# Kernel tuning notes

Measured on AMD Instinct MI355X. Metric: run time of the kernel, lower is better.

## Reference

```python
import jax, jax.numpy as jnp
import numpy as np

N_NODES = 50000
N_EDGES = 600000
HIDDEN = 128
INNER = 256


def _sage_pool(x, src, dst, Wp, bp, Wl, bl, Wr):
    # GraphSAGE 'pool' aggregator: max_j ReLU(W_pool x_j + b_pool) over in-neighbors,
    # then lin_l(aggregated) + lin_r(x_i). lin_l carries the bias (PyG convention).
    m = jax.nn.relu(x[src] @ Wp.T + bp)                      # [E, H] gather + transform
    agg = jax.ops.segment_max(m, dst, num_segments=x.shape[0])  # [N, H] scatter-max
    agg = jnp.where(jnp.isfinite(agg), agg, 0.0)             # isolated nodes -> 0
    return agg @ Wl.T + bl + x @ Wr.T


def setup_inputs() -> dict:
    key = jax.random.key(0)
    ks = jax.random.split(key, 16)
    s_h = 1.0 / np.sqrt(HIDDEN)
    x = jax.random.normal(ks[0], (N_NODES, HIDDEN), dtype=jnp.float32)
    edge_index = jax.random.randint(ks[1], (2, N_EDGES), 0, N_NODES, dtype=jnp.int64)
    p = {}
    # sage1
    p["Wp1"] = jax.random.normal(ks[2], (HIDDEN, HIDDEN), jnp.float32) * s_h
    p["bp1"] = jnp.zeros((HIDDEN,), jnp.float32)
    p["Wl1"] = jax.random.normal(ks[3], (HIDDEN, HIDDEN), jnp.float32) * s_h
    p["bl1"] = jnp.zeros((HIDDEN,), jnp.float32)
    p["Wr1"] = jax.random.normal(ks[4], (HIDDEN, HIDDEN), jnp.float32) * s_h
    # sage2
    p["Wp2"] = jax.random.normal(ks[5], (HIDDEN, HIDDEN), jnp.float32) * s_h
    p["bp2"] = jnp.zeros((HIDDEN,), jnp.float32)
    p["Wl2"] = jax.random.normal(ks[6], (HIDDEN, HIDDEN), jnp.float32) * s_h
    p["bl2"] = jnp.zeros((HIDDEN,), jnp.float32)
    p["Wr2"] = jax.random.normal(ks[7], (HIDDEN, HIDDEN), jnp.float32) * s_h
    # final linear hidden -> inner
    p["Wlin"] = jax.random.normal(ks[8], (INNER, HIDDEN), jnp.float32) * s_h
    p["blin"] = jnp.zeros((INNER,), jnp.float32)
    return {"x": x, "edge_index": edge_index, **p}


def reference(x, edge_index, Wp1, bp1, Wl1, bl1, Wr1, Wp2, bp2, Wl2, bl2, Wr2, Wlin, blin):
    src, dst = edge_index[0], edge_index[1]
    h = _sage_pool(x, src, dst, Wp1, bp1, Wl1, bl1, Wr1)
    h = jax.nn.gelu(h)
    h = _sage_pool(h, src, dst, Wp2, bp2, Wl2, bl2, Wr2)
    h = jax.nn.gelu(h)
    h = jax.nn.gelu(h @ Wlin.T + blin)
    return (h, edge_index)
```

## Files before the change

### kernel.cpp

```cpp
#include <hip/hip_runtime.h>

#define N_NODES 50000
#define N_EDGES 600000
#define HID 128

typedef __attribute__((ext_vector_type(8))) short short8;
typedef __attribute__((ext_vector_type(4))) float f32x4;

__device__ __forceinline__ unsigned short f2bf(float f) {
    unsigned u = __float_as_uint(f);
    unsigned r = u + 0x7FFFu + ((u >> 16) & 1u);
    return (unsigned short)(r >> 16);
}
__device__ __forceinline__ float bf2f(unsigned short h) {
    return __uint_as_float(((unsigned)h) << 16);
}

__device__ __forceinline__ float gelu_fast(float x) {
    float u = 0.7978845608028654f * (x + 0.044715f * x * x * x);
    return x / (1.0f + __expf(-2.0f * u));
}

__global__ void zero_deg(int* __restrict__ zbase) {
    int i = blockIdx.x * 256 + threadIdx.x;
    if (i < 12501) ((int4*)zbase)[i] = make_int4(0, 0, 0, 0);
}

#define CNT_BLOCKS  2344
#define CVT_BLOCKS  3125
#define PACK_BLOCKS 512
__global__ void prep(const float* __restrict__ x, unsigned short* __restrict__ xbf,
                     const float* __restrict__ Wp1, const float* __restrict__ Wl1,
                     const float* __restrict__ Wr1, const float* __restrict__ Wp2,
                     const float* __restrict__ Wl2, const float* __restrict__ Wr2,
                     const float* __restrict__ Wlin, unsigned short* __restrict__ wpack,
                     const int* __restrict__ ei, int* __restrict__ deg,
                     int* __restrict__ rank) {
    int b = blockIdx.x;
    if (b < CNT_BLOCKS) {
        int e = b * 256 + threadIdx.x;
        if (e < N_EDGES) {
            int dst = ei[N_EDGES + e];
            rank[e] = atomicAdd(&deg[dst], 1);
        }
    } else if (b < CNT_BLOCKS + CVT_BLOCKS) {
        int tid = (b - CNT_BLOCKS) * 256 + threadIdx.x;
        size_t i8 = (size_t)tid * 8;
        if (i8 >= (size_t)N_NODES * HID) return;
        float4 v0 = *(const float4*)(x + i8);
        float4 v1 = *(const float4*)(x + i8 + 4);
        short8 o;
        o[0] = f2bf(v0.x); o[1] = f2bf(v0.y); o[2] = f2bf(v0.z); o[3] = f2bf(v0.w);
        o[4] = f2bf(v1.x); o[5] = f2bf(v1.y); o[6] = f2bf(v1.z); o[7] = f2bf(v1.w);
        *(short8*)(xbf + i8) = o;
    } else {
        int pb = b - CNT_BLOCKS - CVT_BLOCKS;
        const float* W;
        int base, idx;
        if (pb < 384) {
            int which = pb >> 6;
            switch (which) {
                case 0: W = Wp1; break;
                case 1: W = Wl1; break;
                case 2: W = Wr1; break;
                case 3: W = Wp2; break;
                case 4: W = Wl2; break;
                default: W = Wr2; break;
            }
            base = which * 16384;
            idx = (pb & 63) * 256 + threadIdx.x;
        } else {
            W = Wlin;
            base = 98304;
            idx = (pb - 384) * 256 + threadIdx.x;
        }
        int j = idx & 7;
        int lane = (idx >> 3) & 63;
        int ks = (idx >> 9) & 3;
        int nt = idx >> 11;
        int c = nt * 16 + (lane & 15);
        int k = ks * 32 + (lane >> 4) * 8 + j;
        wpack[base + idx] = f2bf(W[c * 128 + k]);
    }
}

__global__ void build_off(const int* __restrict__ deg, int* __restrict__ off,
                          int* __restrict__ cursor) {
    __shared__ int sm[256];
    __shared__ int base;
    int t = threadIdx.x;
    int i = blockIdx.x * 256 + t;
    int v = (i < N_NODES) ? deg[i] : 0;
    sm[t] = v;
    __syncthreads();
    for (int s = 1; s < 256; s <<= 1) {
        int tv = (t >= s) ? sm[t - s] : 0;
        __syncthreads();
        sm[t] += tv;
        __syncthreads();
    }
    if (t == 255) base = atomicAdd(cursor, sm[255]);
    __syncthreads();
    if (i < N_NODES) off[i] = base + sm[t] - v;
}

#define FB   2344
#define EB4  1172
#define LB   1563
__global__ __launch_bounds__(256, 2) void combo(
        const int* __restrict__ ei, const int* __restrict__ off,
        const int* __restrict__ rank, int* __restrict__ csr,
        float* __restrict__ echo,
        const unsigned short* __restrict__ in1, const unsigned short* __restrict__ B1,
        const float* __restrict__ bias1, unsigned short* __restrict__ out1) {
    int b = blockIdx.x;
    int t = threadIdx.x;
    if (b < FB) {
        int e = b * 256 + t;
        if (e < N_EDGES) {
            int dst = ei[N_EDGES + e];
            csr[off[dst] + rank[e]] = ei[e];
        }
        return;
    }
    if (b < FB + EB4) {
        int idx = (b - FB) * 256 + t;
        int i = idx * 4;
        if (i < 2 * N_EDGES) {
            int4 v = *(const int4*)(ei + i);
            float4 f = make_float4((float)v.x, (float)v.y, (float)v.z, (float)v.w);
            *(float4*)(echo + i) = f;
        }
        return;
    }
    {
        __shared__ alignas(16) unsigned short hA[32][128];
        const int bid = b - FB - EB4;
        const int w = t >> 6;
        const int l = t & 63;
        const int blockRow = bid * 32;

        int r0 = blockRow + (l & 15);
        int r1 = r0 + 16;
        if (r0 > N_NODES - 1) r0 = N_NODES - 1;
        if (r1 > N_NODES - 1) r1 = N_NODES - 1;
        const int ko = (l >> 4) * 8;

        short8 a1[2][4];
#pragma unroll
        for (int ks = 0; ks < 4; ++ks) {
            a1[0][ks] = *(const short8*)(in1 + (size_t)r0 * HID + ks * 32 + ko);
            a1[1][ks] = *(const short8*)(in1 + (size_t)r1 * HID + ks * 32 + ko);
        }
        const int cL = l & 15;
        const int rfrag = (l >> 4) * 4;

        short8 b1v[8];
        const size_t gb = (size_t)(w * 8) * 64 + l;
#pragma unroll
        for (int s = 0; s < 8; ++s)
            b1v[s] = *(const short8*)(B1 + (gb + (size_t)s * 64) * 8);

#pragma unroll
        for (int m = 0; m < 2; ++m) {
            const int nt = w * 2 + m;
            f32x4 acc0 = {0.f, 0.f, 0.f, 0.f};
            f32x4 acc1 = {0.f, 0.f, 0.f, 0.f};
#pragma unroll
            for (int ks = 0; ks < 4; ++ks) {
                const int step = m * 4 + ks;
                acc0 = __builtin_amdgcn_mfma_f32_16x16x32_bf16(a1[0][ks], b1v[step], acc0, 0, 0, 0);
                acc1 = __builtin_amdgcn_mfma_f32_16x16x32_bf16(a1[1][ks], b1v[step], acc1, 0, 0, 0);
            }
            float bc = bias1[nt * 16 + cL];
#pragma unroll
            for (int reg = 0; reg < 4; ++reg) {
                int rl = rfrag + reg;
                int cs = (nt * 16 + cL) ^ ((rl & 7) << 3);
                hA[rl][cs] = f2bf(acc0[reg] + bc);
                hA[rl + 16][cs] = f2bf(acc1[reg] + bc);
            }
        }
        __syncthreads();
#pragma unroll
        for (int p = 0; p < 2; ++p) {
            int idx = p * 256 + t;
            int row = idx >> 4;
            int c0 = (idx & 15) * 8;
            int cs0 = c0 ^ ((row & 7) << 3);
            short8 v = *(const short8*)&hA[row][cs0];
            int grow = blockRow + row;
            if (grow < N_NODES)
                *(short8*)(out1 + (size_t)grow * HID + c0) = v;
        }
    }
}

template <bool STORE1, int NT2, int ACT2, bool OBF2>
__global__ __launch_bounds__(256, 2) void mfma_fused(
        const unsigned short* __restrict__ in1, const unsigned short* __restrict__ in2,
        const unsigned short* __restrict__ B1, const unsigned short* __restrict__ B2,
        const float* __restrict__ bias1, void* __restrict__ out1,
        const unsigned short* __restrict__ B3, const float* __restrict__ bias3,
        void* __restrict__ out2) {
    __shared__ alignas(16) unsigned short hA[32][128];
    __shared__ alignas(16) unsigned short hB[OBF2 ? 32 : 1][128];
    __shared__ alignas(16) float fT[OBF2 ? 1 : 32][260];

    const int t = threadIdx.x;
    const int w = t >> 6;
    const int l = t & 63;
    const int blockRow = blockIdx.x * 32;

    int r0 = blockRow + (l & 15);
    int r1 = r0 + 16;
    if (r0 > N_NODES - 1) r0 = N_NODES - 1;
    if (r1 > N_NODES - 1) r1 = N_NODES - 1;
    const int ko = (l >> 4) * 8;

    short8 a1[2][4], a2[2][4];
#pragma unroll
    for (int ks = 0; ks < 4; ++ks) {
        a1[0][ks] = *(const short8*)(in1 + (size_t)r0 * HID + ks * 32 + ko);
        a1[1][ks] = *(const short8*)(in1 + (size_t)r1 * HID + ks * 32 + ko);
        a2[0][ks] = *(const short8*)(in2 + (size_t)r0 * HID + ks * 32 + ko);
        a2[1][ks] = *(const short8*)(in2 + (size_t)r1 * HID + ks * 32 + ko);
    }
    const int cL = l & 15;
    const int rfrag = (l >> 4) * 4;

    {
        short8 b1v[8], b2v[8];
        const size_t gb = (size_t)(w * 8) * 64 + l;
#pragma unroll
        for (int s = 0; s < 8; ++s) {
            b1v[s] = *(const short8*)(B1 + (gb + (size_t)s * 64) * 8);
            b2v[s] = *(const short8*)(B2 + (gb + (size_t)s * 64) * 8);
        }
#pragma unroll
        for (int m = 0; m < 2; ++m) {
            const int nt = w * 2 + m;
            f32x4 acc0 = {0.f, 0.f, 0.f, 0.f};
            f32x4 acc1 = {0.f, 0.f, 0.f, 0.f};
#pragma unroll
            for (int ks = 0; ks < 4; ++ks) {
                const int step = m * 4 + ks;
                acc0 = __builtin_amdgcn_mfma_f32_16x16x32_bf16(a1[0][ks], b1v[step], acc0, 0, 0, 0);
                acc1 = __builtin_amdgcn_mfma_f32_16x16x32_bf16(a1[1][ks], b1v[step], acc1, 0, 0, 0);
                acc0 = __builtin_amdgcn_mfma_f32_16x16x32_bf16(a2[0][ks], b2v[step], acc0, 0, 0, 0);
                acc1 = __builtin_amdgcn_mfma_f32_16x16x32_bf16(a2[1][ks], b2v[step], acc1, 0, 0, 0);
            }
            float bc = bias1[nt * 16 + cL];
#pragma unroll
            for (int reg = 0; reg < 4; ++reg) {
                float v0 = gelu_fast(acc0[reg] + bc);
                float v1 = gelu_fast(acc1[reg] + bc);
                int rl = rfrag + reg;
                int cs = (nt * 16 + cL) ^ ((rl & 7) << 3);
                hA[rl][cs] = f2bf(v0);
                hA[rl + 16][cs] = f2bf(v1);
            }
        }
    }
    __syncthreads();

    if (STORE1) {
#pragma unroll
        for (int p = 0; p < 2; ++p) {
            int idx = p * 256 + t;
            int row = idx >> 4;
            int c0 = (idx & 15) * 8;
            int cs0 = c0 ^ ((row & 7) << 3);
            short8 v = *(const short8*)&hA[row][cs0];
            int grow = blockRow + row;
            if (grow < N_NODES)
                *(short8*)((unsigned short*)out1 + (size_t)grow * HID + c0) = v;
        }
    }

    short8 c1[2][4];
    const int rA = l & 15;
#pragma unroll
    for (int ks = 0; ks < 4; ++ks) {
        int b0 = (ks * 32 + ko) ^ ((rA & 7) << 3);
        c1[0][ks] = *(const short8*)&hA[rA][b0];
        c1[1][ks] = *(const short8*)&hA[rA + 16][b0];
    }
    if (OBF2) {
        short8 b1v[8];
        const size_t gb = (size_t)(w * 8) * 64 + l;
#pragma unroll
        for (int s = 0; s < 8; ++s)
            b1v[s] = *(const short8*)(B3 + (gb + (size_t)s * 64) * 8);
#pragma unroll
        for (int m = 0; m < 2; ++m) {
            const int nt = w * 2 + m;
            f32x4 acc0 = {0.f, 0.f, 0.f, 0.f};
            f32x4 acc1 = {0.f, 0.f, 0.f, 0.f};
#pragma unroll
            for (int ks = 0; ks < 4; ++ks) {
                const int step = m * 4 + ks;
                acc0 = __builtin_amdgcn_mfma_f32_16x16x32_bf16(c1[0][ks], b1v[step], acc0, 0, 0, 0);
                acc1 = __builtin_amdgcn_mfma_f32_16x16x32_bf16(c1[1][ks], b1v[step], acc1, 0, 0, 0);
            }
            float bc = bias3[nt * 16 + cL];
#pragma unroll
            for (int reg = 0; reg < 4; ++reg) {
                float v0 = acc0[reg] + bc;
                float v1 = acc1[reg] + bc;
                if (ACT2 == 1) { v0 = gelu_fast(v0); v1 = gelu_fast(v1); }
                int rl = rfrag + reg;
                int cs = (nt * 16 + cL) ^ ((rl & 7) << 3);
                hB[rl][cs] = f2bf(v0);
                hB[rl + 16][cs] = f2bf(v1);
            }
        }
        __syncthreads();
#pragma unroll
        for (int p = 0; p < 2; ++p) {
            int idx = p * 256 + t;
            int row = idx >> 4;
            int c0 = (idx & 15) * 8;
            int cs0 = c0 ^ ((row & 7) << 3);
            short8 v = *(const short8*)&hB[row][cs0];
            int grow = blockRow + row;
            if (grow < N_NODES)
                *(short8*)((unsigned short*)out2 + (size_t)grow * (NT2 * 16) + c0) = v;
        }
    } else {
        short8 b1v[16];
        const size_t gb0 = (size_t)(w * 8) * 64 + l;
        const size_t gb1 = (size_t)(32 + w * 8) * 64 + l;
#pragma unroll
        for (int s = 0; s < 8; ++s) {
            b1v[s] = *(const short8*)(B3 + (gb0 + (size_t)s * 64) * 8);
            b1v[8 + s] = *(const short8*)(B3 + (gb1 + (size_t)s * 64) * 8);
        }
#pragma unroll
        for (int mi = 0; mi < 4; ++mi) {
            const int nt = (mi < 2) ? (w * 2 + mi) : (8 + w * 2 + (mi - 2));
            f32x4 acc0 = {0.f, 0.f, 0.f, 0.f};
            f32x4 acc1 = {0.f, 0.f, 0.f, 0.f};
#pragma unroll
            for (int ks = 0; ks < 4; ++ks) {
                const int step = mi * 4 + ks;
                acc0 = __builtin_amdgcn_mfma_f32_16x16x32_bf16(c1[0][ks], b1v[step], acc0, 0, 0, 0);
                acc1 = __builtin_amdgcn_mfma_f32_16x16x32_bf16(c1[1][ks], b1v[step], acc1, 0, 0, 0);
            }
            float bc = bias3[nt * 16 + cL];
            int ct = nt * 16 + cL;
#pragma unroll
            for (int reg = 0; reg < 4; ++reg) {
                float v0 = acc0[reg] + bc;
                float v1 = acc1[reg] + bc;
                if (ACT2 == 1) { v0 = gelu_fast(v0); v1 = gelu_fast(v1); }
                fT[rfrag + reg][ct] = v0;
                fT[rfrag + reg + 16][ct] = v1;
            }
        }
        __syncthreads();
#pragma unroll
        for (int p = 0; p < 8; ++p) {
            int idx = p * 256 + t;
            int row = idx >> 6;
            int s4 = (idx & 63) * 4;
            float4 v = *(const float4*)&fT[row][s4];
            int grow = blockRow + row;
            if (grow < N_NODES)
                *(float4*)((float*)out2 + (size_t)grow * 256 + s4) = v;
        }
    }
}

__global__ __launch_bounds__(256) void seg_max_bf(const unsigned short* __restrict__ y,
                                                  const int* __restrict__ csr,
                                                  const int* __restrict__ off,
                                                  const int* __restrict__ deg,
                                                  unsigned short* __restrict__ agg) {
    int n = blockIdx.x * 4 + (threadIdx.x >> 6);
    int lane = threadIdx.x & 63;
    int s = off[n];
    int d = deg[n];
    const unsigned short* yb = y + lane * 2;
    float a0 = 0.f, a1 = 0.f;
    int i = 0;
    for (; i + 4 <= d; i += 4) {
        int s0 = csr[s + i], s1 = csr[s + i + 1], s2 = csr[s + i + 2], s3 = csr[s + i + 3];
        unsigned v0 = *(const unsigned*)(yb + (size_t)s0 * HID);
        unsigned v1 = *(const unsigned*)(yb + (size_t)s1 * HID);
        unsigned v2 = *(const unsigned*)(yb + (size_t)s2 * HID);
        unsigned v3 = *(const unsigned*)(yb + (size_t)s3 * HID);
        a0 = fmaxf(a0, fmaxf(fmaxf(__uint_as_float(v0 << 16), __uint_as_float(v1 << 16)),
                             fmaxf(__uint_as_float(v2 << 16), __uint_as_float(v3 << 16))));
        a1 = fmaxf(a1, fmaxf(fmaxf(__uint_as_float(v0 & 0xffff0000u), __uint_as_float(v1 & 0xffff0000u)),
                             fmaxf(__uint_as_float(v2 & 0xffff0000u), __uint_as_float(v3 & 0xffff0000u))));
    }
    for (; i < d; ++i) {
        int s0 = csr[s + i];
        unsigned v0 = *(const unsigned*)(yb + (size_t)s0 * HID);
        a0 = fmaxf(a0, __uint_as_float(v0 << 16));
        a1 = fmaxf(a1, __uint_as_float(v0 & 0xffff0000u));
    }
    unsigned o = (unsigned)f2bf(a0) | ((unsigned)f2bf(a1) << 16);
    *(unsigned*)(agg + (size_t)n * HID + lane * 2) = o;
}

extern "C" void kernel_launch(void* const* d_in, const int* in_sizes, int n_in,
                              void* d_out, int out_size, void* d_ws, size_t ws_size,
                              hipStream_t stream) {
    const float* x    = (const float*)d_in[0];
    const int*   ei   = (const int*)d_in[1];
    const float* Wp1  = (const float*)d_in[2];
    const float* bp1  = (const float*)d_in[3];
    const float* Wl1  = (const float*)d_in[4];
    const float* bl1  = (const float*)d_in[5];
    const float* Wr1  = (const float*)d_in[6];
    const float* Wp2  = (const float*)d_in[7];
    const float* bp2  = (const float*)d_in[8];
    const float* Wl2  = (const float*)d_in[9];
    const float* bl2  = (const float*)d_in[10];
    const float* Wr2  = (const float*)d_in[11];
    const float* Wlin = (const float*)d_in[12];
    const float* blin = (const float*)d_in[13];
    float* out = (float*)d_out;

    unsigned short* wpack = (unsigned short*)d_ws;
    unsigned short* xbf   = wpack + 131072;
    unsigned short* ybf   = xbf + (size_t)N_NODES * HID;
    unsigned short* aggbf = ybf + (size_t)N_NODES * HID;
    unsigned short* h1bf  = aggbf + (size_t)N_NODES * HID;
    int* deg    = (int*)(h1bf + (size_t)N_NODES * HID);
    int* cursor = deg + N_NODES;
    int* off    = cursor + 4;
    int* rank   = off + N_NODES;
    int* csr    = rank + N_EDGES;

    const unsigned short* Bp1 = wpack + 0;
    const unsigned short* Bl1 = wpack + 16384;
    const unsigned short* Br1 = wpack + 32768;
    const unsigned short* Bp2 = wpack + 49152;
    const unsigned short* Bl2 = wpack + 65536;
    const unsigned short* Br2 = wpack + 81920;
    const unsigned short* Blin = wpack + 98304;

    const int RB32 = (N_NODES + 31) / 32;
    const int NPB  = (N_NODES + 255) / 256;

    hipLaunchKernelGGL(zero_deg, dim3(49), dim3(256), 0, stream, deg);

    hipLaunchKernelGGL(prep, dim3(CNT_BLOCKS + CVT_BLOCKS + PACK_BLOCKS), dim3(256), 0, stream,
                       x, xbf, Wp1, Wl1, Wr1, Wp2, Wl2, Wr2, Wlin, wpack, ei, deg, rank);

    hipLaunchKernelGGL(build_off, dim3(NPB), dim3(256), 0, stream, deg, off, cursor);

    hipLaunchKernelGGL(combo, dim3(FB + EB4 + LB), dim3(256), 0, stream,
                       ei, off, rank, csr, out + (size_t)N_NODES * 256,
                       xbf, Bp1, bp1, ybf);

    hipLaunchKernelGGL(seg_max_bf, dim3(N_NODES / 4), dim3(256), 0, stream,
                       ybf, csr, off, deg, aggbf);

    hipLaunchKernelGGL((mfma_fused<true, 8, 0, true>), dim3(RB32), dim3(256), 0, stream,
                       aggbf, xbf, Bl1, Br1, bl1, h1bf, Bp2, bp2, ybf);

    hipLaunchKernelGGL(seg_max_bf, dim3(N_NODES / 4), dim3(256), 0, stream,
                       ybf, csr, off, deg, aggbf);

    hipLaunchKernelGGL((mfma_fused<false, 16, 1, false>), dim3(RB32), dim3(256), 0, stream,
                       aggbf, h1bf, Bl2, Br2, bl2, nullptr, Blin, blin, out);
}
```

Measured before the change: 179.3 us.

## Precompute root-term lin_r projections alongside pool transforms, store bf16 residuals

After: 170.9 us. 1.05x faster.

```diff
diff --git a/kernel.cpp b/kernel.cpp
--- a/kernel.cpp
+++ b/kernel.cpp
@@ -26,7 +26,7 @@
     if (i < 12501) ((int4*)zbase)[i] = make_int4(0, 0, 0, 0);
 }
 
-#define CNT_BLOCKS  2344
+#define CNT_BLOCKS  1172
 #define CVT_BLOCKS  3125
 #define PACK_BLOCKS 512
 __global__ void prep(const float* __restrict__ x, unsigned short* __restrict__ xbf,
@@ -38,10 +38,14 @@
                      int* __restrict__ rank) {
     int b = blockIdx.x;
     if (b < CNT_BLOCKS) {
-        int e = b * 256 + threadIdx.x;
-        if (e < N_EDGES) {
-            int dst = ei[N_EDGES + e];
-            rank[e] = atomicAdd(&deg[dst], 1);
+        int e = b * 512 + threadIdx.x;
+#pragma unroll
+        for (int q = 0; q < 2; ++q) {
+            int ee = e + q * 256;
+            if (ee < N_EDGES) {
+                int dst = ei[N_EDGES + ee];
+                rank[ee] = atomicAdd(&deg[dst], 1);
+            }
         }
     } else if (b < CNT_BLOCKS + CVT_BLOCKS) {
         int tid = (b - CNT_BLOCKS) * 256 + threadIdx.x;
@@ -104,7 +108,7 @@
     if (i < N_NODES) off[i] = base + sm[t] - v;
 }
 
-#define FB   2344
+#define FB2  1172
 #define EB4  1172
 #define LB   1563
 __global__ __launch_bounds__(256, 2) void combo(
@@ -112,19 +116,24 @@
         const int* __restrict__ rank, int* __restrict__ csr,
         float* __restrict__ echo,
         const unsigned short* __restrict__ in1, const unsigned short* __restrict__ B1,
-        const float* __restrict__ bias1, unsigned short* __restrict__ out1) {
+        const unsigned short* __restrict__ B2, const float* __restrict__ bias1,
+        unsigned short* __restrict__ out1, unsigned short* __restrict__ rout) {
     int b = blockIdx.x;
     int t = threadIdx.x;
-    if (b < FB) {
-        int e = b * 256 + t;
-        if (e < N_EDGES) {
-            int dst = ei[N_EDGES + e];
-            csr[off[dst] + rank[e]] = ei[e];
+    if (b < FB2) {
+        int e = b * 512 + t;
+#pragma unroll
+        for (int q = 0; q < 2; ++q) {
+            int ee = e + q * 256;
+            if (ee < N_EDGES) {
+                int dst = ei[N_EDGES + ee];
+                csr[off[dst] + rank[ee]] = ei[ee];
+            }
         }
         return;
     }
-    if (b < FB + EB4) {
-        int idx = (b - FB) * 256 + t;
+    if (b < FB2 + EB4) {
+        int idx = (b - FB2) * 256 + t;
         int i = idx * 4;
         if (i < 2 * N_EDGES) {
             int4 v = *(const int4*)(ei + i);
@@ -135,7 +144,8 @@
     }
     {
         __shared__ alignas(16) unsigned short hA[32][128];
-        const int bid = b - FB - EB4;
+        __shared__ alignas(16) unsigned short hR[32][128];
+        const int bid = b - FB2 - EB4;
         const int w = t >> 6;
         const int l = t & 63;
         const int blockRow = bid * 32;
@@ -155,22 +165,28 @@
         const int cL = l & 15;
         const int rfrag = (l >> 4) * 4;
 
-        short8 b1v[8];
+        short8 b1v[8], b2v[8];
         const size_t gb = (size_t)(w * 8) * 64 + l;
 #pragma unroll
-        for (int s = 0; s < 8; ++s)
+        for (int s = 0; s < 8; ++s) {
             b1v[s] = *(const short8*)(B1 + (gb + (size_t)s * 64) * 8);
+            b2v[s] = *(const short8*)(B2 + (gb + (size_t)s * 64) * 8);
+        }
 
 #pragma unroll
         for (int m = 0; m < 2; ++m) {
             const int nt = w * 2 + m;
             f32x4 acc0 = {0.f, 0.f, 0.f, 0.f};
             f32x4 acc1 = {0.f, 0.f, 0.f, 0.f};
+            f32x4 acc2 = {0.f, 0.f, 0.f, 0.f};
+            f32x4 acc3 = {0.f, 0.f, 0.f, 0.f};
 #pragma unroll
             for (int ks = 0; ks < 4; ++ks) {
                 const int step = m * 4 + ks;
                 acc0 = __builtin_amdgcn_mfma_f32_16x16x32_bf16(a1[0][ks], b1v[step], acc0, 0, 0, 0);
                 acc1 = __builtin_amdgcn_mfma_f32_16x16x32_bf16(a1[1][ks], b1v[step], acc1, 0, 0, 0);
+                acc2 = __builtin_amdgcn_mfma_f32_16x16x32_bf16(a1[0][ks], b2v[step], acc2, 0, 0, 0);
+                acc3 = __builtin_amdgcn_mfma_f32_16x16x32_bf16(a1[1][ks], b2v[step], acc3, 0, 0, 0);
             }
             float bc = bias1[nt * 16 + cL];
 #pragma unroll
@@ -179,6 +195,8 @@
                 int cs = (nt * 16 + cL) ^ ((rl & 7) << 3);
                 hA[rl][cs] = f2bf(acc0[reg] + bc);
                 hA[rl + 16][cs] = f2bf(acc1[reg] + bc);
+                hR[rl][cs] = f2bf(acc2[reg]);
+                hR[rl + 16][cs] = f2bf(acc3[reg]);
             }
         }
         __syncthreads();
@@ -189,28 +207,43 @@
             int c0 = (idx & 15) * 8;
             int cs0 = c0 ^ ((row & 7) << 3);
             short8 v = *(const short8*)&hA[row][cs0];
+            short8 vr = *(const short8*)&hR[row][cs0];
             int grow = blockRow + row;
-            if (grow < N_NODES)
+            if (grow < N_NODES) {
                 *(short8*)(out1 + (size_t)grow * HID + c0) = v;
-        }
-    }
-}
-
-template <bool STORE1, int NT2, int ACT2, bool OBF2>
+                *(short8*)(rout + (size_t)grow * HID + c0) = vr;
+            }
+        }
+    }
+}
+
+template <bool DUALOUT, int ACT2>
 __global__ __launch_bounds__(256, 2) void mfma_fused(
-        const unsigned short* __restrict__ in1, const unsigned short* __restrict__ in2,
-        const unsigned short* __restrict__ B1, const unsigned short* __restrict__ B2,
-        const float* __restrict__ bias1, void* __restrict__ out1,
+        const unsigned short* __restrict__ in1, const unsigned short* __restrict__ radd,
+        const unsigned short* __restrict__ B1, const float* __restrict__ bias1,
         const unsigned short* __restrict__ B3, const float* __restrict__ bias3,
-        void* __restrict__ out2) {
+        void* __restrict__ out3,
+        const unsigned short* __restrict__ B4, unsigned short* __restrict__ out4) {
+    __shared__ alignas(16) unsigned short rT[32][136];
     __shared__ alignas(16) unsigned short hA[32][128];
-    __shared__ alignas(16) unsigned short hB[OBF2 ? 32 : 1][128];
-    __shared__ alignas(16) float fT[OBF2 ? 1 : 32][260];
+    __shared__ alignas(16) unsigned short hB[DUALOUT ? 32 : 1][128];
+    __shared__ alignas(16) unsigned short hR[DUALOUT ? 32 : 1][128];
+    __shared__ alignas(16) float fT[DUALOUT ? 1 : 32][260];
 
     const int t = threadIdx.x;
     const int w = t >> 6;
     const int l = t & 63;
     const int blockRow = blockIdx.x * 32;
+
+#pragma unroll
+    for (int p = 0; p < 2; ++p) {
+        int idx = p * 256 + t;
+        int row = idx >> 4;
+        int c0 = (idx & 15) * 8;
+        int grow = blockRow + row;
+        if (grow > N_NODES - 1) grow = N_NODES - 1;
+        *(short8*)&rT[row][c0] = *(const short8*)(radd + (size_t)grow * HID + c0);
+    }
 
     int r0 = blockRow + (l & 15);
     int r1 = r0 + 16;
@@ -218,25 +251,23 @@
     if (r1 > N_NODES - 1) r1 = N_NODES - 1;
     const int ko = (l >> 4) * 8;
 
-    short8 a1[2][4], a2[2][4];
+    short8 a1[2][4];
 #pragma unroll
     for (int ks = 0; ks < 4; ++ks) {
         a1[0][ks] = *(const short8*)(in1 + (size_t)r0 * HID + ks * 32 + ko);
         a1[1][ks] = *(const short8*)(in1 + (size_t)r1 * HID + ks * 32 + ko);
-        a2[0][ks] = *(const short8*)(in2 + (size_t)r0 * HID + ks * 32 + ko);
-        a2[1][ks] = *(const short8*)(in2 + (size_t)r1 * HID + ks * 32 + ko);
     }
     const int cL = l & 15;
     const int rfrag = (l >> 4) * 4;
 
+    __syncthreads();
+
     {
-        short8 b1v[8], b2v[8];
+        short8 b1v[8];
         const size_t gb = (size_t)(w * 8) * 64 + l;
 #pragma unroll
-        for (int s = 0; s < 8; ++s) {
+        for (int s = 0; s < 8; ++s)
             b1v[s] = *(const short8*)(B1 + (gb + (size_t)s * 64) * 8);
-            b2v[s] = *(const short8*)(B2 + (gb + (size_t)s * 64) * 8);
-        }
 #pragma unroll
         for (int m = 0; m < 2; ++m) {
             const int nt = w * 2 + m;
@@ -247,36 +278,21 @@
                 const int step = m * 4 + ks;
                 acc0 = __builtin_amdgcn_mfma_f32_16x16x32_bf16(a1[0][ks], b1v[step], acc0, 0, 0, 0);
                 acc1 = __builtin_amdgcn_mfma_f32_16x16x32_bf16(a1[1][ks], b1v[step], acc1, 0, 0, 0);
-                acc0 = __builtin_amdgcn_mfma_f32_16x16x32_bf16(a2[0][ks], b2v[step], acc0, 0, 0, 0);
-                acc1 = __builtin_amdgcn_mfma_f32_16x16x32_bf16(a2[1][ks], b2v[step], acc1, 0, 0, 0);
             }
             float bc = bias1[nt * 16 + cL];
+            int ct = nt * 16 + cL;
 #pragma unroll
             for (int reg = 0; reg < 4; ++reg) {
-                float v0 = gelu_fast(acc0[reg] + bc);
-                float v1 = gelu_fast(acc1[reg] + bc);
                 int rl = rfrag + reg;
-                int cs = (nt * 16 + cL) ^ ((rl & 7) << 3);
+                float v0 = gelu_fast(acc0[reg] + bc + bf2f(rT[rl][ct]));
+                float v1 = gelu_fast(acc1[reg] + bc + bf2f(rT[rl + 16][ct]));
+                int cs = ct ^ ((rl & 7) << 3);
                 hA[rl][cs] = f2bf(v0);
                 hA[rl + 16][cs] = f2bf(v1);
             }
         }
     }
     __syncthreads();
-
-    if (STORE1) {
-#pragma unroll
-        for (int p = 0; p < 2; ++p) {
-            int idx = p * 256 + t;
-            int row = idx >> 4;
-            int c0 = (idx & 15) * 8;
-            int cs0 = c0 ^ ((row & 7) << 3);
-            short8 v = *(const short8*)&hA[row][cs0];
-            int grow = blockRow + row;
-            if (grow < N_NODES)
-                *(short8*)((unsigned short*)out1 + (size_t)grow * HID + c0) = v;
-        }
-    }
 
     short8 c1[2][4];
     const int rA = l & 15;
@@ -286,33 +302,38 @@
         c1[0][ks] = *(const short8*)&hA[rA][b0];
         c1[1][ks] = *(const short8*)&hA[rA + 16][b0];
     }
-    if (OBF2) {
-        short8 b1v[8];
+    if (DUALOUT) {
+        short8 b3v[8], b4v[8];
         const size_t gb = (size_t)(w * 8) * 64 + l;
 #pragma unroll
-        for (int s = 0; s < 8; ++s)
-            b1v[s] = *(const short8*)(B3 + (gb + (size_t)s * 64) * 8);
+        for (int s = 0; s < 8; ++s) {
+            b3v[s] = *(const short8*)(B3 + (gb + (size_t)s * 64) * 8);
+            b4v[s] = *(const short8*)(B4 + (gb + (size_t)s * 64) * 8);
+        }
 #pragma unroll
         for (int m = 0; m < 2; ++m) {
             const int nt = w * 2 + m;
-            f32x4 acc0 = {0.f, 0.f, 0.f, 0.f};
-            f32x4 acc1 = {0.f, 0.f, 0.f, 0.f};
+            f32x4 accP0 = {0.f, 0.f, 0.f, 0.f};
+            f32x4 accP1 = {0.f, 0.f, 0.f, 0.f};
+            f32x4 accR0 = {0.f, 0.f, 0.f, 0.f};
+            f32x4 accR1 = {0.f, 0.f, 0.f, 0.f};
 #pragma unroll
             for (int ks = 0; ks < 4; ++ks) {
                 const int step = m * 4 + ks;
-                acc0 = __builtin_amdgcn_mfma_f32_16x16x32_bf16(c1[0][ks], b1v[step], acc0, 0, 0, 0);
-                acc1 = __builtin_amdgcn_mfma_f32_16x16x32_bf16(c1[1][ks], b1v[step], acc1, 0, 0, 0);
+                accP0 = __builtin_amdgcn_mfma_f32_16x16x32_bf16(c1[0][ks], b3v[step], accP0, 0, 0, 0);
+                accP1 = __builtin_amdgcn_mfma_f32_16x16x32_bf16(c1[1][ks], b3v[step], accP1, 0, 0, 0);
+                accR0 = __builtin_amdgcn_mfma_f32_16x16x32_bf16(c1[0][ks], b4v[step], accR0, 0, 0, 0);
+                accR1 = __builtin_amdgcn_mfma_f32_16x16x32_bf16(c1[1][ks], b4v[step], accR1, 0, 0, 0);
             }
             float bc = bias3[nt * 16 + cL];
 #pragma unroll
             for (int reg = 0; reg < 4; ++reg) {
-                float v0 = acc0[reg] + bc;
-                float v1 = acc1[reg] + bc;
-                if (ACT2 == 1) { v0 = gelu_fast(v0); v1 = gelu_fast(v1); }
                 int rl = rfrag + reg;
                 int cs = (nt * 16 + cL) ^ ((rl & 7) << 3);
-                hB[rl][cs] = f2bf(v0);
-                hB[rl + 16][cs] = f2bf(v1);
+                hB[rl][cs] = f2bf(accP0[reg] + bc);
+                hB[rl + 16][cs] = f2bf(accP1[reg] + bc);
+                hR[rl][cs] = f2bf(accR0[reg]);
+                hR[rl + 16][cs] = f2bf(accR1[reg]);
             }
         }
         __syncthreads();
@@ -323,9 +344,12 @@
             int c0 = (idx & 15) * 8;
             int cs0 = c0 ^ ((row & 7) << 3);
             short8 v = *(const short8*)&hB[row][cs0];
+            short8 vr = *(const short8*)&hR[row][cs0];
             int grow = blockRow + row;
-            if (grow < N_NODES)
-                *(short8*)((unsigned short*)out2 + (size_t)grow * (NT2 * 16) + c0) = v;
+            if (grow < N_NODES) {
+                *(short8*)((unsigned short*)out3 + (size_t)grow * HID + c0) = v;
+                *(short8*)(out4 + (size_t)grow * HID + c0) = vr;
+            }
         }
     } else {
         short8 b1v[16];
@@ -367,7 +391,7 @@
             float4 v = *(const float4*)&fT[row][s4];
             int grow = blockRow + row;
             if (grow < N_NODES)
-                *(float4*)((float*)out2 + (size_t)grow * 256 + s4) = v;
+                *(float4*)((float*)out3 + (size_t)grow * 256 + s4) = v;
         }
     }
 }
@@ -428,8 +452,9 @@
     unsigned short* xbf   = wpack + 131072;
     unsigned short* ybf   = xbf + (size_t)N_NODES * HID;
     unsigned short* aggbf = ybf + (size_t)N_NODES * HID;
-    unsigned short* h1bf  = aggbf + (size_t)N_NODES * HID;
-    int* deg    = (int*)(h1bf + (size_t)N_NODES * HID);
+    unsigned short* r1bf  = aggbf + (size_t)N_NODES * HID;
+    unsigned short* r2bf  = r1bf + (size_t)N_NODES * HID;
+    int* deg    = (int*)(r2bf + (size_t)N_NODES * HID);
     int* cursor = deg + N_NODES;
     int* off    = cursor + 4;
     int* rank   = off + N_NODES;
@@ -453,19 +478,19 @@
 
     hipLaunchKernelGGL(build_off, dim3(NPB), dim3(256), 0, stream, deg, off, cursor);
 
-    hipLaunchKernelGGL(combo, dim3(FB + EB4 + LB), dim3(256), 0, stream,
+    hipLaunchKernelGGL(combo, dim3(FB2 + EB4 + LB), dim3(256), 0, stream,
                        ei, off, rank, csr, out + (size_t)N_NODES * 256,
-                       xbf, Bp1, bp1, ybf);
+                       xbf, Bp1, Br1, bp1, ybf, r1bf);
 
     hipLaunchKernelGGL(seg_max_bf, dim3(N_NODES / 4), dim3(256), 0, stream,
                        ybf, csr, off, deg, aggbf);
 
-    hipLaunchKernelGGL((mfma_fused<true, 8, 0, true>), dim3(RB32), dim3(256), 0, stream,
-                       aggbf, xbf, Bl1, Br1, bl1, h1bf, Bp2, bp2, ybf);
+    hipLaunchKernelGGL((mfma_fused<true, 0>), dim3(RB32), dim3(256), 0, stream,
+                       aggbf, r1bf, Bl1, bl1, Bp2, bp2, ybf, Br2, r2bf);
 
     hipLaunchKernelGGL(seg_max_bf, dim3(N_NODES / 4), dim3(256), 0, stream,
                        ybf, csr, off, deg, aggbf);
 
-    hipLaunchKernelGGL((mfma_fused<false, 16, 1, false>), dim3(RB32), dim3(256), 0, stream,
-                       aggbf, h1bf, Bl2, Br2, bl2, nullptr, Blin, blin, out);
-}
+    hipLaunchKernelGGL((mfma_fused<false, 1>), dim3(RB32), dim3(256), 0, stream,
+                       aggbf, r2bf, Bl2, bl2, Blin, blin, out, nullptr, nullptr);
+}
```
